# Optimization experiments

Hardware: AMD Instinct MI355X
Metric: run time of the kernel (lower is better)

The kernel has to match this reference:

```python
import jax, jax.numpy as jnp
import numpy as np


def setup_inputs() -> dict:
    key = jax.random.key(0)
    ks = jax.random.split(key, 6)
    B, I, H, O = 4096, 2048, 2048, 2048
    return {
        "x": jax.random.normal(ks[0], (B, I), dtype=jnp.float32),
        "hidden": jax.random.normal(ks[1], (B, H), dtype=jnp.float32),
        "W_ih": jax.random.normal(ks[2], (H, I + H), dtype=jnp.float32) * (1.0 / np.sqrt(I + H)),
        "b_ih": jax.random.normal(ks[3], (H,), dtype=jnp.float32) * 0.01,
        "W_ho": jax.random.normal(ks[4], (O, H), dtype=jnp.float32) * (1.0 / np.sqrt(H)),
        "b_ho": jax.random.normal(ks[5], (O,), dtype=jnp.float32) * 0.01,
    }


def reference(x, hidden, W_ih, b_ih, W_ho, b_ho):
    # Fused RNN cell:
    #   combined   = [x, hidden]                      [B, I+H]
    #   new_hidden = tanh(combined @ W_ih^T + b_ih)   [B, H]
    #   output     = new_hidden @ W_ho^T + b_ho       [B, O]
    combined = jnp.concatenate([x, hidden], axis=-1)
    new_hidden = jnp.tanh(jnp.einsum('bk,hk->bh', combined, W_ih) + b_ih)
    output = jnp.einsum('bh,oh->bo', new_hidden, W_ho) + b_ho
    return output, new_hidden
```

## Files before the change

kernel.cpp:

```cpp
#include <hip/hip_runtime.h>
#include <hip/hip_bf16.h>

typedef unsigned short u16;
typedef __attribute__((ext_vector_type(8))) __bf16 bf16x8;
typedef __attribute__((ext_vector_type(4))) float f32x4;

#define AS1 __attribute__((address_space(1)))
#define AS3 __attribute__((address_space(3)))

__device__ __forceinline__ u16 f2bf(float f) {
    union { float f; unsigned u; } v; v.f = f;
    unsigned u = v.u;
    return (u16)((u + 0x7FFFu + ((u >> 16) & 1u)) >> 16);
}

__global__ void cvt4(const float4* __restrict__ a, const float4* __restrict__ b,
                     const float4* __restrict__ c, const float4* __restrict__ d,
                     ushort4* __restrict__ oa, ushort4* __restrict__ ob,
                     ushort4* __restrict__ oc, ushort4* __restrict__ od,
                     int na, int nb, int nc, int nd) {
    const int total = na + nb + nc + nd;
    for (int i = blockIdx.x * blockDim.x + threadIdx.x; i < total;
         i += gridDim.x * blockDim.x) {
        const float4* s; ushort4* o; int j = i;
        if (j < na) { s = a; o = oa; }
        else {
            j -= na;
            if (j < nb) { s = b; o = ob; }
            else {
                j -= nb;
                if (j < nc) { s = c; o = oc; }
                else        { j -= nc; s = d; o = od; }
            }
        }
        float4 v = s[j];
        ushort4 u;
        u.x = f2bf(v.x); u.y = f2bf(v.y); u.z = f2bf(v.z); u.w = f2bf(v.w);
        o[j] = u;
    }
}

template<int MODE>
__global__ __launch_bounds__(512, 2)
void gemm_bt(const u16* __restrict__ A0, const u16* __restrict__ A1,
             const u16* __restrict__ Bm, const float* __restrict__ bias,
             float* __restrict__ Cf, u16* __restrict__ Cbf,
             int M, int N, int K)
{
    extern __shared__ u16 lds[];
    const int tid  = threadIdx.x;
    const int wave = tid >> 6;
    const int lane = tid & 63;

    const int nN  = N >> 7;
    const int nwg = (M >> 8) * nN;
    const int id  = ((int)blockIdx.x % 8) * (nwg >> 3) + (int)blockIdx.x / 8;
    const int m0  = (id / nN) << 8;
    const int n0  = (id % nN) << 7;

    const int fr = lane & 15, fq = lane >> 4;
    const int wr = wave >> 1, wc = wave & 1;

    const int srow   = tid >> 3;
    const int schunk = (tid & 7) ^ (srow & 7);
    const int ldsW   = wave << 9;

    f32x4 acc[4][4];
    #pragma unroll
    for (int i = 0; i < 4; ++i)
        #pragma unroll
        for (int j = 0; j < 4; ++j)
            acc[i][j] = f32x4{0.f, 0.f, 0.f, 0.f};

    const int lda = (MODE == 0) ? 2048 : K;

    auto stage = [&](int t) {
        const int k0  = t << 6;
        const int buf = (t % 3) * 24576;
        const u16* As; int kc;
        if constexpr (MODE == 0) { As = (k0 < 2048) ? A0 : A1; kc = k0 & 2047; }
        else                     { As = A0;                    kc = k0;        }
        #pragma unroll
        for (int r = 0; r < 4; ++r) {
            const u16* g = As + (size_t)(m0 + (r << 6) + srow) * lda + kc + (schunk << 3);
            __builtin_amdgcn_global_load_lds((const AS1 unsigned int*)g,
                (AS3 unsigned int*)&lds[buf + (r << 12) + ldsW], 16, 0, 0);
        }
        #pragma unroll
        for (int r = 0; r < 2; ++r) {
            const u16* g = Bm + (size_t)(n0 + (r << 6) + srow) * K + k0 + (schunk << 3);
            __builtin_amdgcn_global_load_lds((const AS1 unsigned int*)g,
                (AS3 unsigned int*)&lds[buf + 16384 + (r << 12) + ldsW], 16, 0, 0);
        }
    };

    const int ax0 = ((fq)     ^ (fr & 7)) << 3;
    const int ax1 = ((4 + fq) ^ (fr & 7)) << 3;
    const int aoff = ((wr << 6) + fr) << 6;
    const int boff = ((wc << 6) + fr) << 6;

    const int nt = K >> 6;

    stage(0); stage(1);
    asm volatile("s_waitcnt vmcnt(6)" ::: "memory");
    __builtin_amdgcn_s_barrier();

    for (int t = 0; t < nt; ++t) {
        const int buf = (t % 3) * 24576;
        if (t + 2 < nt) stage(t + 2);

        bf16x8 a0[4], a1[4], b0[4], b1[4];
        #pragma unroll
        for (int i = 0; i < 4; ++i) {
            a0[i] = *(const bf16x8*)&lds[buf + aoff + (i << 10) + ax0];
            a1[i] = *(const bf16x8*)&lds[buf + aoff + (i << 10) + ax1];
        }
        #pragma unroll
        for (int j = 0; j < 4; ++j) {
            b0[j] = *(const bf16x8*)&lds[buf + 16384 + boff + (j << 10) + ax0];
            b1[j] = *(const bf16x8*)&lds[buf + 16384 + boff + (j << 10) + ax1];
        }

        __builtin_amdgcn_s_setprio(1);
        #pragma unroll
        for (int i = 0; i < 4; ++i)
            #pragma unroll
            for (int j = 0; j < 4; ++j) {
                acc[i][j] = __builtin_amdgcn_mfma_f32_16x16x32_bf16(a0[i], b0[j], acc[i][j], 0, 0, 0);
                acc[i][j] = __builtin_amdgcn_mfma_f32_16x16x32_bf16(a1[i], b1[j], acc[i][j], 0, 0, 0);
            }
        __builtin_amdgcn_s_setprio(0);

        if (t + 1 < nt) {
            if (t + 2 < nt) asm volatile("s_waitcnt vmcnt(6)" ::: "memory");
            else            asm volatile("s_waitcnt vmcnt(0)" ::: "memory");
            __builtin_amdgcn_s_barrier();
        }
    }

    #pragma unroll
    for (int j = 0; j < 4; ++j) {
        const int col = n0 + (wc << 6) + (j << 4) + fr;
        const float bv = bias[col];
        #pragma unroll
        for (int i = 0; i < 4; ++i) {
            #pragma unroll
            for (int r = 0; r < 4; ++r) {
                const int row = m0 + (wr << 6) + (i << 4) + (fq << 2) + r;
                float v = acc[i][j][r] + bv;
                if constexpr (MODE == 0) {
                    v = tanhf(v);
                    Cf[(size_t)row * N + col]  = v;
                    Cbf[(size_t)row * N + col] = f2bf(v);
                } else {
                    Cf[(size_t)row * N + col] = v;
                }
            }
        }
    }
}

extern "C" void kernel_launch(void* const* d_in, const int* in_sizes, int n_in,
                              void* d_out, int out_size, void* d_ws, size_t ws_size,
                              hipStream_t stream) {
    const float* x   = (const float*)d_in[0];
    const float* hid = (const float*)d_in[1];
    const float* Wih = (const float*)d_in[2];
    const float* bih = (const float*)d_in[3];
    const float* Who = (const float*)d_in[4];
    const float* bho = (const float*)d_in[5];
    float* out = (float*)d_out;

    const int B = 4096, I = 2048, H = 2048, O = 2048;

    u16* x_bf   = (u16*)d_ws;
    u16* h_bf   = x_bf   + (size_t)B * I;
    u16* wih_bf = h_bf   + (size_t)B * H;
    u16* who_bf = wih_bf + (size_t)H * (I + H);
    u16* nh_bf  = who_bf + (size_t)O * H;

    const int na = (B * I) / 4, nb = (B * H) / 4,
              nc = (H * (I + H)) / 4, nd = (O * H) / 4;
    cvt4<<<dim3(2048), dim3(256), 0, stream>>>(
        (const float4*)x, (const float4*)hid, (const float4*)Wih, (const float4*)Who,
        (ushort4*)x_bf, (ushort4*)h_bf, (ushort4*)wih_bf, (ushort4*)who_bf,
        na, nb, nc, nd);

    float* out_y  = out;
    float* out_nh = out + (size_t)B * O;

    const size_t shmem = 3 * 24576 * sizeof(u16);
    hipFuncSetAttribute(reinterpret_cast<const void*>(&gemm_bt<0>),
                        hipFuncAttributeMaxDynamicSharedMemorySize, (int)shmem);
    hipFuncSetAttribute(reinterpret_cast<const void*>(&gemm_bt<1>),
                        hipFuncAttributeMaxDynamicSharedMemorySize, (int)shmem);

    gemm_bt<0><<<dim3((B / 256) * (H / 128)), dim3(512), shmem, stream>>>(
        x_bf, h_bf, wih_bf, bih, out_nh, nh_bf, B, H, I + H);

    gemm_bt<1><<<dim3((B / 256) * (O / 128)), dim3(512), shmem, stream>>>(
        nh_bf, nh_bf, who_bf, bho, out_y, nullptr, B, O, H);
}
```

Measured before the change: 289.9 us.

## Interleave LDS reads, global prefetch and MFMA in four phased quadrant stages

Each K-step of the main loop is split into four quadrant phases. Each phase reads only the A/B fragments it needs from LDS, issues part of the next-next tile's global-to-LDS loads, then runs its MFMAs, with barriers and setprio between phases. The aim is to overlap LDS reads and global prefetch issue with matrix-core work and to lower register pressure. The cost is several extra workgroup barriers per iteration, which may stall waves and cut the natural overlap between the two resident workgroups.

```diff
diff --git a/kernel.cpp b/kernel.cpp
--- a/kernel.cpp
+++ b/kernel.cpp
@@ -74,23 +74,27 @@
 
     const int lda = (MODE == 0) ? 2048 : K;
 
-    auto stage = [&](int t) {
+    auto stage_part = [&](int t, int part) {
         const int k0  = t << 6;
         const int buf = (t % 3) * 24576;
-        const u16* As; int kc;
-        if constexpr (MODE == 0) { As = (k0 < 2048) ? A0 : A1; kc = k0 & 2047; }
-        else                     { As = A0;                    kc = k0;        }
-        #pragma unroll
-        for (int r = 0; r < 4; ++r) {
-            const u16* g = As + (size_t)(m0 + (r << 6) + srow) * lda + kc + (schunk << 3);
-            __builtin_amdgcn_global_load_lds((const AS1 unsigned int*)g,
-                (AS3 unsigned int*)&lds[buf + (r << 12) + ldsW], 16, 0, 0);
-        }
-        #pragma unroll
-        for (int r = 0; r < 2; ++r) {
-            const u16* g = Bm + (size_t)(n0 + (r << 6) + srow) * K + k0 + (schunk << 3);
-            __builtin_amdgcn_global_load_lds((const AS1 unsigned int*)g,
-                (AS3 unsigned int*)&lds[buf + 16384 + (r << 12) + ldsW], 16, 0, 0);
+        if (part < 2) {
+            const u16* As; int kc;
+            if constexpr (MODE == 0) { As = (k0 < 2048) ? A0 : A1; kc = k0 & 2047; }
+            else                     { As = A0;                    kc = k0;        }
+            #pragma unroll
+            for (int rr = 0; rr < 2; ++rr) {
+                const int r = part * 2 + rr;
+                const u16* g = As + (size_t)(m0 + (r << 6) + srow) * lda + kc + (schunk << 3);
+                __builtin_amdgcn_global_load_lds((const AS1 unsigned int*)g,
+                    (AS3 unsigned int*)&lds[buf + (r << 12) + ldsW], 16, 0, 0);
+            }
+        } else {
+            #pragma unroll
+            for (int r = 0; r < 2; ++r) {
+                const u16* g = Bm + (size_t)(n0 + (r << 6) + srow) * K + k0 + (schunk << 3);
+                __builtin_amdgcn_global_load_lds((const AS1 unsigned int*)g,
+                    (AS3 unsigned int*)&lds[buf + 16384 + (r << 12) + ldsW], 16, 0, 0);
+            }
         }
     };
 
@@ -101,39 +105,89 @@
 
     const int nt = K >> 6;
 
-    stage(0); stage(1);
+    stage_part(0, 0); stage_part(0, 1); stage_part(0, 2);
+    stage_part(1, 0); stage_part(1, 1); stage_part(1, 2);
     asm volatile("s_waitcnt vmcnt(6)" ::: "memory");
     __builtin_amdgcn_s_barrier();
 
     for (int t = 0; t < nt; ++t) {
         const int buf = (t % 3) * 24576;
-        if (t + 2 < nt) stage(t + 2);
-
-        bf16x8 a0[4], a1[4], b0[4], b1[4];
-        #pragma unroll
-        for (int i = 0; i < 4; ++i) {
-            a0[i] = *(const bf16x8*)&lds[buf + aoff + (i << 10) + ax0];
-            a1[i] = *(const bf16x8*)&lds[buf + aoff + (i << 10) + ax1];
-        }
-        #pragma unroll
-        for (int j = 0; j < 4; ++j) {
-            b0[j] = *(const bf16x8*)&lds[buf + 16384 + boff + (j << 10) + ax0];
-            b1[j] = *(const bf16x8*)&lds[buf + 16384 + boff + (j << 10) + ax1];
-        }
-
-        __builtin_amdgcn_s_setprio(1);
-        #pragma unroll
-        for (int i = 0; i < 4; ++i)
-            #pragma unroll
-            for (int j = 0; j < 4; ++j) {
-                acc[i][j] = __builtin_amdgcn_mfma_f32_16x16x32_bf16(a0[i], b0[j], acc[i][j], 0, 0, 0);
-                acc[i][j] = __builtin_amdgcn_mfma_f32_16x16x32_bf16(a1[i], b1[j], acc[i][j], 0, 0, 0);
+        const bool pf = (t + 2 < nt);
+
+        bf16x8 aL[2][2], aH[2][2], bL[2][2], bH[2][2];
+
+        #pragma unroll
+        for (int i = 0; i < 2; ++i) {
+            aL[i][0] = *(const bf16x8*)&lds[buf + aoff + (i << 10) + ax0];
+            aL[i][1] = *(const bf16x8*)&lds[buf + aoff + (i << 10) + ax1];
+            bL[i][0] = *(const bf16x8*)&lds[buf + 16384 + boff + (i << 10) + ax0];
+            bL[i][1] = *(const bf16x8*)&lds[buf + 16384 + boff + (i << 10) + ax1];
+        }
+        if (pf) stage_part(t + 2, 0);
+        __builtin_amdgcn_s_barrier();
+        asm volatile("s_waitcnt lgkmcnt(0)" ::: "memory");
+        __builtin_amdgcn_s_setprio(1);
+        #pragma unroll
+        for (int i = 0; i < 2; ++i)
+            #pragma unroll
+            for (int j = 0; j < 2; ++j) {
+                acc[i][j] = __builtin_amdgcn_mfma_f32_16x16x32_bf16(aL[i][0], bL[j][0], acc[i][j], 0, 0, 0);
+                acc[i][j] = __builtin_amdgcn_mfma_f32_16x16x32_bf16(aL[i][1], bL[j][1], acc[i][j], 0, 0, 0);
+            }
+        __builtin_amdgcn_s_setprio(0);
+        __builtin_amdgcn_s_barrier();
+
+        #pragma unroll
+        for (int j = 0; j < 2; ++j) {
+            bH[j][0] = *(const bf16x8*)&lds[buf + 16384 + boff + ((j + 2) << 10) + ax0];
+            bH[j][1] = *(const bf16x8*)&lds[buf + 16384 + boff + ((j + 2) << 10) + ax1];
+        }
+        if (pf) stage_part(t + 2, 1);
+        __builtin_amdgcn_s_barrier();
+        asm volatile("s_waitcnt lgkmcnt(0)" ::: "memory");
+        __builtin_amdgcn_s_setprio(1);
+        #pragma unroll
+        for (int i = 0; i < 2; ++i)
+            #pragma unroll
+            for (int j = 0; j < 2; ++j) {
+                acc[i][j + 2] = __builtin_amdgcn_mfma_f32_16x16x32_bf16(aL[i][0], bH[j][0], acc[i][j + 2], 0, 0, 0);
+                acc[i][j + 2] = __builtin_amdgcn_mfma_f32_16x16x32_bf16(aL[i][1], bH[j][1], acc[i][j + 2], 0, 0, 0);
+            }
+        __builtin_amdgcn_s_setprio(0);
+        __builtin_amdgcn_s_barrier();
+
+        #pragma unroll
+        for (int i = 0; i < 2; ++i) {
+            aH[i][0] = *(const bf16x8*)&lds[buf + aoff + ((i + 2) << 10) + ax0];
+            aH[i][1] = *(const bf16x8*)&lds[buf + aoff + ((i + 2) << 10) + ax1];
+        }
+        __builtin_amdgcn_s_barrier();
+        asm volatile("s_waitcnt lgkmcnt(0)" ::: "memory");
+        __builtin_amdgcn_s_setprio(1);
+        #pragma unroll
+        for (int i = 0; i < 2; ++i)
+            #pragma unroll
+            for (int j = 0; j < 2; ++j) {
+                acc[i + 2][j] = __builtin_amdgcn_mfma_f32_16x16x32_bf16(aH[i][0], bL[j][0], acc[i + 2][j], 0, 0, 0);
+                acc[i + 2][j] = __builtin_amdgcn_mfma_f32_16x16x32_bf16(aH[i][1], bL[j][1], acc[i + 2][j], 0, 0, 0);
+            }
+        __builtin_amdgcn_s_setprio(0);
+        __builtin_amdgcn_s_barrier();
+
+        if (pf) stage_part(t + 2, 2);
+        __builtin_amdgcn_s_setprio(1);
+        #pragma unroll
+        for (int i = 0; i < 2; ++i)
+            #pragma unroll
+            for (int j = 0; j < 2; ++j) {
+                acc[i + 2][j + 2] = __builtin_amdgcn_mfma_f32_16x16x32_bf16(aH[i][0], bH[j][0], acc[i + 2][j + 2], 0, 0, 0);
+                acc[i + 2][j + 2] = __builtin_amdgcn_mfma_f32_16x16x32_bf16(aH[i][1], bH[j][1], acc[i + 2][j + 2], 0, 0, 0);
             }
         __builtin_amdgcn_s_setprio(0);
 
         if (t + 1 < nt) {
-            if (t + 2 < nt) asm volatile("s_waitcnt vmcnt(6)" ::: "memory");
-            else            asm volatile("s_waitcnt vmcnt(0)" ::: "memory");
+            if (pf) asm volatile("s_waitcnt vmcnt(6)" ::: "memory");
+            else    asm volatile("s_waitcnt vmcnt(0)" ::: "memory");
             __builtin_amdgcn_s_barrier();
         }
     }
```

After: 297.6 us. 1.03x slower.
